# Performance work log

Measured on AMD Instinct MI355X. Metric: run time of the kernel, lower is better.

Reference implementation:

```python
import jax, jax.numpy as jnp
import numpy as np

B, L_HIST, N_VARS, L_FUT = 32, 96, 862, 96
D_MODEL, D_INNER, D_STATE, D_CONV, DT_RANK, D_FF, E_LAYERS = 512, 512, 32, 2, 32, 512, 2
EPS = 1e-5


def _ln(x, w, b):
    m = x.mean(-1, keepdims=True)
    v = ((x - m) ** 2).mean(-1, keepdims=True)
    return (x - m) * jax.lax.rsqrt(v + EPS) * w + b


def _mamba(x, in_w, conv_w, conv_b, x_w, dt_w, dt_b, A_log, D, out_w):
    # x: [B, T, d_model]; standard mamba-ssm selective-scan block (inference)
    Bb, T, _ = x.shape
    u, z = jnp.split(x @ in_w, 2, axis=-1)                      # [B,T,E] each
    uc = jnp.transpose(u, (0, 2, 1))                            # [B,E,T]
    uc = jax.lax.conv_general_dilated(
        uc, conv_w[:, None, :], (1,), [(D_CONV - 1, 0)],
        dimension_numbers=('NCH', 'OIH', 'NCH'),
        feature_group_count=D_INNER)                            # causal depthwise conv
    u = jax.nn.silu(jnp.transpose(uc, (0, 2, 1)) + conv_b)      # [B,T,E]
    dt, Bm, Cm = jnp.split(u @ x_w, [DT_RANK, DT_RANK + D_STATE], axis=-1)
    delta = jax.nn.softplus(dt @ dt_w + dt_b)                   # [B,T,E]
    A = -jnp.exp(A_log)                                         # [E,S]

    def step(h, inp):
        d_t, u_t, B_t, C_t = inp                                # [B,E],[B,E],[B,S],[B,S]
        h = jnp.exp(d_t[..., None] * A) * h + (d_t * u_t)[..., None] * B_t[:, None, :]
        return h, jnp.einsum('bes,bs->be', h, C_t)

    h0 = jnp.zeros((Bb, D_INNER, D_STATE), x.dtype)
    _, ys = jax.lax.scan(step, h0, (delta.transpose(1, 0, 2), u.transpose(1, 0, 2),
                                    Bm.transpose(1, 0, 2), Cm.transpose(1, 0, 2)))
    y = ys.transpose(1, 0, 2) + u * D
    return (y * jax.nn.silu(z)) @ out_w


def _forward(history_data, emb_w, emb_b, m_in_w, m_conv_w, m_conv_b, m_x_w,
             m_dt_w, m_dt_b, m_A_log, m_D, m_out_w, ffn_w1, ffn_b1, ffn_w2,
             ffn_b2, norm1_w, norm1_b, norm2_w, norm2_b, normf_w, normf_b,
             proj_w, proj_b):
    x_enc = history_data[..., 0]                                # [B,L,N]
    means = jax.lax.stop_gradient(x_enc.mean(1, keepdims=True))
    x_enc = x_enc - means
    stdev = jnp.sqrt(x_enc.var(axis=1, keepdims=True) + EPS)
    x_enc = x_enc / stdev
    x = jnp.transpose(x_enc, (0, 2, 1)) @ emb_w + emb_b         # [B,N,d_model] (inverted embed)
    for l in range(E_LAYERS):
        fwd = _mamba(x, m_in_w[l, 0], m_conv_w[l, 0], m_conv_b[l, 0], m_x_w[l, 0],
                     m_dt_w[l, 0], m_dt_b[l, 0], m_A_log[l, 0], m_D[l, 0], m_out_w[l, 0])
        rev = _mamba(x[:, ::-1], m_in_w[l, 1], m_conv_w[l, 1], m_conv_b[l, 1], m_x_w[l, 1],
                     m_dt_w[l, 1], m_dt_b[l, 1], m_A_log[l, 1], m_D[l, 1], m_out_w[l, 1])[:, ::-1]
        x = _ln(x + fwd + rev, norm1_w[l], norm1_b[l])
        y = jax.nn.relu(x @ ffn_w1[l] + ffn_b1[l]) @ ffn_w2[l] + ffn_b2[l]
        x = _ln(x + y, norm2_w[l], norm2_b[l])
    x = _ln(x, normf_w, normf_b)
    dec = jnp.transpose(x @ proj_w + proj_b, (0, 2, 1))         # [B,L_FUT,N]
    dec = dec * stdev[:, 0][:, None, :] + means[:, 0][:, None, :]
    return dec[..., None]                                       # [B,L_FUT,N,1]


def setup_inputs() -> dict:
    key = jax.random.key(0)
    ks = jax.random.split(key, 16)
    def rn(k, shape, s=0.02):
        return jax.random.normal(k, shape, jnp.float32) * s
    M = (E_LAYERS, 2)
    inp = {}
    inp['history_data'] = jax.random.normal(ks[0], (B, L_HIST, N_VARS, 1), jnp.float32)
    inp['emb_w'] = rn(ks[1], (L_HIST, D_MODEL))
    inp['emb_b'] = jnp.zeros((D_MODEL,), jnp.float32)
    inp['m_in_w'] = rn(ks[2], M + (D_MODEL, 2 * D_INNER))
    inp['m_conv_w'] = rn(ks[3], M + (D_INNER, D_CONV), 0.1)
    inp['m_conv_b'] = jnp.zeros(M + (D_INNER,), jnp.float32)
    inp['m_x_w'] = rn(ks[4], M + (D_INNER, DT_RANK + 2 * D_STATE))
    inp['m_dt_w'] = rn(ks[5], M + (DT_RANK, D_INNER), 0.1)
    inp['m_dt_b'] = jnp.full(M + (D_INNER,), -4.0, jnp.float32)
    a = jnp.log(jnp.arange(1, D_STATE + 1, dtype=jnp.float32))
    inp['m_A_log'] = jnp.broadcast_to(a, M + (D_INNER, D_STATE))
    inp['m_D'] = jnp.ones(M + (D_INNER,), jnp.float32)
    inp['m_out_w'] = rn(ks[6], M + (D_INNER, D_MODEL))
    inp['ffn_w1'] = rn(ks[7], (E_LAYERS, D_MODEL, D_FF))
    inp['ffn_b1'] = jnp.zeros((E_LAYERS, D_FF), jnp.float32)
    inp['ffn_w2'] = rn(ks[8], (E_LAYERS, D_FF, D_MODEL))
    inp['ffn_b2'] = jnp.zeros((E_LAYERS, D_MODEL), jnp.float32)
    inp['norm1_w'] = jnp.ones((E_LAYERS, D_MODEL), jnp.float32)
    inp['norm1_b'] = jnp.zeros((E_LAYERS, D_MODEL), jnp.float32)
    inp['norm2_w'] = jnp.ones((E_LAYERS, D_MODEL), jnp.float32)
    inp['norm2_b'] = jnp.zeros((E_LAYERS, D_MODEL), jnp.float32)
    inp['normf_w'] = jnp.ones((D_MODEL,), jnp.float32)
    inp['normf_b'] = jnp.zeros((D_MODEL,), jnp.float32)
    inp['proj_w'] = rn(ks[9], (D_MODEL, L_FUT))
    inp['proj_b'] = jnp.zeros((L_FUT,), jnp.float32)
    return inp


def reference(history_data, emb_w, emb_b, m_in_w, m_conv_w, m_conv_b, m_x_w,
              m_dt_w, m_dt_b, m_A_log, m_D, m_out_w, ffn_w1, ffn_b1, ffn_w2,
              ffn_b2, norm1_w, norm1_b, norm2_w, norm2_b, normf_w, normf_b,
              proj_w, proj_b):
    return _forward(history_data, emb_w, emb_b, m_in_w, m_conv_w, m_conv_b, m_x_w,
                    m_dt_w, m_dt_b, m_A_log, m_D, m_out_w, ffn_w1, ffn_b1, ffn_w2,
                    ffn_b2, norm1_w, norm1_b, norm2_w, norm2_b, normf_w, normf_b,
                    proj_w, proj_b)
```

## Files before the change

### kernel.cpp

```cpp
#include <hip/hip_runtime.h>
#include <math.h>

#define BATCH 32
#define LHIST 96
#define NVARS 862
#define LFUT  96
#define DMODEL 512
#define DINNER 512
#define DSTATE 32
#define DTRANK 32
#define SCAN_C 32
#define SCAN_TC ((NVARS + SCAN_C - 1) / SCAN_C)

typedef short short8 __attribute__((ext_vector_type(8)));
typedef float floatx4 __attribute__((ext_vector_type(4)));
typedef unsigned short ushort;

#define LOG2E 1.44269504088896f

static __device__ __forceinline__ ushort f2b(float f) {
    unsigned u = __builtin_bit_cast(unsigned, f);
    unsigned r = (u + 0x7FFFu + ((u >> 16) & 1u)) >> 16;
    return (ushort)r;
}
static __device__ __forceinline__ float b2f(ushort h) {
    unsigned u = ((unsigned)h) << 16;
    return __builtin_bit_cast(float, u);
}

static __device__ __forceinline__ void load_lds16(const void* g, void* l) {
    __builtin_amdgcn_global_load_lds(
        (const __attribute__((address_space(1))) unsigned int*)g,
        (__attribute__((address_space(3))) unsigned int*)l, 16, 0, 0);
}

__global__ void meanstd_k(const float* __restrict__ hist, ushort* __restrict__ xinb,
                          float* __restrict__ meanb, float* __restrict__ stdb,
                          int b0, int CB) {
    int idx = blockIdx.x * blockDim.x + threadIdx.x;
    if (idx >= CB * NVARS) return;
    int b = b0 + idx / NVARS, n = idx % NVARS;
    const float* p = hist + (size_t)b * LHIST * NVARS + n;
    float s = 0.f;
    for (int l = 0; l < LHIST; l++) s += p[(size_t)l * NVARS];
    float mean = s * (1.f / LHIST);
    float v = 0.f;
    for (int l = 0; l < LHIST; l++) { float d = p[(size_t)l * NVARS] - mean; v += d * d; }
    v *= (1.f / LHIST);
    float sd = sqrtf(v + 1e-5f);
    float inv = 1.f / sd;
    meanb[idx] = mean;
    stdb[idx]  = sd;
    ushort* o = xinb + (size_t)idx * LHIST;
    for (int l = 0; l < LHIST; l++) o[l] = f2b((p[(size_t)l * NVARS] - mean) * inv);
}

__global__ void castT_k(const float* __restrict__ W, ushort* __restrict__ Wt,
                        int K, int N, int P) {
    size_t idx = (size_t)blockIdx.x * blockDim.x + threadIdx.x;
    if (idx >= (size_t)P * K * N) return;
    size_t kn = (size_t)K * N;
    int p = (int)(idx / kn);
    int rem = (int)(idx % kn);
    int k = rem / N, n = rem % N;
    Wt[(size_t)p * kn + (size_t)n * K + k] = f2b(W[idx]);
}

#define TBM 128
#define TBN 128
#define TBK 32

__global__ __launch_bounds__(256)
void bgemm_k(const ushort* __restrict__ A, int lda,
             const ushort* __restrict__ Bt, int ldb,
             const float* __restrict__ bias,
             float* __restrict__ C, int ldc,
             ushort* __restrict__ C2, int ldc2,
             int M, int N, int K, int act, int accum) {
    __shared__ ushort As[TBM][TBK];
    __shared__ ushort Bs[TBN][TBK];
    int tid = threadIdx.x;
    int gm0 = blockIdx.y * TBM, gn0 = blockIdx.x * TBN;
    int lane = tid & 63, w = tid >> 6;
    int wm = (w >> 1) * 64, wn = (w & 1) * 64;
    int col16 = lane & 15, quad = lane >> 4;

    floatx4 acc[4][4];
#pragma unroll
    for (int i = 0; i < 4; i++)
#pragma unroll
        for (int j = 0; j < 4; j++) acc[i][j] = (floatx4){0.f, 0.f, 0.f, 0.f};

    int srow = tid >> 2;
    int schunk = (tid & 3) * 8;

    const ushort* pa0 = A + (size_t)min(gm0 + srow, M - 1) * lda + schunk;
    const ushort* pa1 = A + (size_t)min(gm0 + srow + 64, M - 1) * lda + schunk;
    const ushort* pb0 = Bt + (size_t)min(gn0 + srow, N - 1) * ldb + schunk;
    const ushort* pb1 = Bt + (size_t)min(gn0 + srow + 64, N - 1) * ldb + schunk;
    ushort* la0 = &As[0][0] + (size_t)tid * 8;
    ushort* la1 = la0 + 2048;
    ushort* lb0 = &Bs[0][0] + (size_t)tid * 8;
    ushort* lb1 = lb0 + 2048;

    for (int k0 = 0; k0 < K; k0 += TBK) {
        __syncthreads();
        load_lds16(pa0 + k0, la0);
        load_lds16(pa1 + k0, la1);
        load_lds16(pb0 + k0, lb0);
        load_lds16(pb1 + k0, lb1);
        __syncthreads();

        short8 af[4], bf[4];
#pragma unroll
        for (int mt = 0; mt < 4; mt++)
            af[mt] = *(const short8*)&As[wm + mt * 16 + col16][quad * 8];
#pragma unroll
        for (int nt = 0; nt < 4; nt++)
            bf[nt] = *(const short8*)&Bs[wn + nt * 16 + col16][quad * 8];
#pragma unroll
        for (int mt = 0; mt < 4; mt++)
#pragma unroll
            for (int nt = 0; nt < 4; nt++)
                acc[mt][nt] = __builtin_amdgcn_mfma_f32_16x16x32_bf16(
                    af[mt], bf[nt], acc[mt][nt], 0, 0, 0);
    }

    int rbase = gm0 + wm + quad * 4;
    int cbase = gn0 + wn + col16;
#pragma unroll
    for (int mt = 0; mt < 4; mt++) {
#pragma unroll
        for (int reg = 0; reg < 4; reg++) {
            int r = rbase + mt * 16 + reg;
            if (r >= M) continue;
#pragma unroll
            for (int nt = 0; nt < 4; nt++) {
                int c = cbase + nt * 16;
                if (c >= N) continue;
                float v = acc[mt][nt][reg];
                if (bias) v += bias[c];
                if (act == 1) v = fmaxf(v, 0.f);
                else if (act == 2) v = (v > 20.f) ? v : log1pf(expf(v));
                if (accum) v += C[(size_t)r * ldc + c];
                if (C)  C[(size_t)r * ldc + c] = v;
                if (C2) C2[(size_t)r * ldc2 + c] = f2b(v);
            }
        }
    }
}

__global__ void conv8_k(const ushort* __restrict__ uzb, const float* __restrict__ cw,
                        const float* __restrict__ cb, ushort* __restrict__ ucb,
                        int rev, int R) {
    int idx = blockIdx.x * blockDim.x + threadIdx.x;
    if (idx >= R * 64) return;
    int m = idx >> 6;
    int e0 = (idx & 63) * 8;
    int t = m % NVARS;
    const ushort* up = uzb + (size_t)m * 1024 + e0;
    short8 cur = *(const short8*)up;
    short8 oth = (short8){0,0,0,0,0,0,0,0};
    if (!rev) { if (t > 0)          oth = *(const short8*)(up - 1024); }
    else      { if (t < NVARS - 1)  oth = *(const short8*)(up + 1024); }
    short8 res;
#pragma unroll
    for (int i = 0; i < 8; i++) {
        int e = e0 + i;
        float v = cw[e * 2] * b2f((ushort)oth[i]) + cw[e * 2 + 1] * b2f((ushort)cur[i]) + cb[e];
        float sig = 1.f / (1.f + __expf(-v));
        res[i] = (short)f2b(v * sig);
    }
    *(short8*)(ucb + (size_t)m * 512 + e0) = res;
}


static __device__ __forceinline__ bool a_is_fast(const float* A_log, int e) {
    bool f = true;
#pragma unroll
    for (int s = 0; s < DSTATE; s++) {
        float a = -__expf(A_log[e * DSTATE + s]);
        f = f && (fabsf(a + (float)(s + 1)) < 1e-3f * (s + 1));
    }
    return f;
}

__global__ __launch_bounds__(256, 4)
void scan_part_k(const ushort* __restrict__ deltab, const ushort* __restrict__ ucb,
                 const float* __restrict__ xdbc, const float* __restrict__ A_log,
                 float* __restrict__ Hpart, float* __restrict__ Sd,
                 int rev, int CB) {
    int NP = CB * DINNER;
    int idx = blockIdx.x * blockDim.x + threadIdx.x;
    if (idx >= NP * SCAN_C) return;
    int c = idx / NP, be = idx % NP;
    int b = be >> 9, e = be & (DINNER - 1);

    float h[DSTATE];
#pragma unroll
    for (int s = 0; s < DSTATE; s++) h[s] = 0.f;
    float sd = 0.f;
    int tau1 = min((c + 1) * SCAN_TC, NVARS);
    if (a_is_fast(A_log, e)) {
        for (int tau = c * SCAN_TC; tau < tau1; tau++) {
            int t = rev ? (NVARS - 1 - tau) : tau;
            size_t m = (size_t)b * NVARS + t;
            float d  = b2f(deltab[m * 512 + e]);
            float uv = b2f(ucb[m * 512 + e]);
            float du = d * uv;
            sd += d;
            const float4* Bp4 = (const float4*)(xdbc + m * 96 + DTRANK);
            float q = __expf(-d), pw = q;
#pragma unroll
            for (int g = 0; g < 8; g++) {
                float4 bv = Bp4[g];
                h[4*g+0] = pw * h[4*g+0] + du * bv.x; pw *= q;
                h[4*g+1] = pw * h[4*g+1] + du * bv.y; pw *= q;
                h[4*g+2] = pw * h[4*g+2] + du * bv.z; pw *= q;
                h[4*g+3] = pw * h[4*g+3] + du * bv.w; if (g < 7) pw *= q;
            }
        }
    } else {
        for (int tau = c * SCAN_TC; tau < tau1; tau++) {
            int t = rev ? (NVARS - 1 - tau) : tau;
            size_t m = (size_t)b * NVARS + t;
            float d  = b2f(deltab[m * 512 + e]);
            float uv = b2f(ucb[m * 512 + e]);
            float du = d * uv;
            sd += d;
            const float* Bp = xdbc + m * 96 + DTRANK;
#pragma unroll
            for (int s = 0; s < DSTATE; s++) {
                float a2 = -__expf(A_log[e * DSTATE + s]) * LOG2E;
                h[s] = exp2f(d * a2) * h[s] + du * Bp[s];
            }
        }
    }
    Sd[(size_t)c * NP + be] = sd;
#pragma unroll
    for (int s = 0; s < DSTATE; s++)
        Hpart[((size_t)c * DSTATE + s) * NP + be] = h[s];
}

__global__ __launch_bounds__(256)
void scan_carry_k(float* __restrict__ Hpart, const float* __restrict__ Sd,
                  const float* __restrict__ A_log, int CB) {
    int NP = CB * DINNER;
    int idx = blockIdx.x * blockDim.x + threadIdx.x;
    if (idx >= NP * DSTATE) return;
    int s = idx / NP, be = idx % NP;
    int e = be & (DINNER - 1);
    float a2 = -__expf(A_log[e * DSTATE + s]) * LOG2E;
    float carry = 0.f;
    for (int c = 0; c < SCAN_C; c++) {
        float sd = Sd[(size_t)c * NP + be];
        size_t off = ((size_t)c * DSTATE + s) * NP + be;
        float hp = Hpart[off];
        Hpart[off] = carry;
        carry = hp + exp2f(a2 * sd) * carry;
    }
}

__global__ __launch_bounds__(256, 4)
void scan_final_k(const ushort* __restrict__ deltab, const ushort* __restrict__ uzb,
                  const ushort* __restrict__ ucb, const float* __restrict__ xdbc,
                  const float* __restrict__ A_log, const float* __restrict__ Dp,
                  const float* __restrict__ CarryIn, ushort* __restrict__ yb,
                  int rev, int CB) {
    int NP = CB * DINNER;
    int idx = blockIdx.x * blockDim.x + threadIdx.x;
    if (idx >= NP * SCAN_C) return;
    int c = idx / NP, be = idx % NP;
    int b = be >> 9, e = be & (DINNER - 1);

    float h[DSTATE];
#pragma unroll
    for (int s = 0; s < DSTATE; s++)
        h[s] = CarryIn[((size_t)c * DSTATE + s) * NP + be];
    float Dv = Dp[e];
    int tau1 = min((c + 1) * SCAN_TC, NVARS);
    if (a_is_fast(A_log, e)) {
        for (int tau = c * SCAN_TC; tau < tau1; tau++) {
            int t = rev ? (NVARS - 1 - tau) : tau;
            size_t m = (size_t)b * NVARS + t;
            float d  = b2f(deltab[m * 512 + e]);
            float zz = b2f(uzb[m * 1024 + 512 + e]);
            float uv = b2f(ucb[m * 512 + e]);
            float du = d * uv;
            const float4* Bp4 = (const float4*)(xdbc + m * 96 + DTRANK);
            const float4* Cp4 = Bp4 + 8;
            float q = __expf(-d), pw = q;
            float accv = 0.f;
#pragma unroll
            for (int g = 0; g < 8; g++) {
                float4 bv = Bp4[g];
                float4 cv = Cp4[g];
                h[4*g+0] = pw * h[4*g+0] + du * bv.x; accv += h[4*g+0] * cv.x; pw *= q;
                h[4*g+1] = pw * h[4*g+1] + du * bv.y; accv += h[4*g+1] * cv.y; pw *= q;
                h[4*g+2] = pw * h[4*g+2] + du * bv.z; accv += h[4*g+2] * cv.z; pw *= q;
                h[4*g+3] = pw * h[4*g+3] + du * bv.w; accv += h[4*g+3] * cv.w;
                if (g < 7) pw *= q;
            }
            float sig = 1.f / (1.f + __expf(-zz));
            yb[m * 512 + e] = f2b((accv + uv * Dv) * (zz * sig));
        }
    } else {
        for (int tau = c * SCAN_TC; tau < tau1; tau++) {
            int t = rev ? (NVARS - 1 - tau) : tau;
            size_t m = (size_t)b * NVARS + t;
            float d  = b2f(deltab[m * 512 + e]);
            float zz = b2f(uzb[m * 1024 + 512 + e]);
            float uv = b2f(ucb[m * 512 + e]);
            float du = d * uv;
            const float* Bp = xdbc + m * 96 + DTRANK;
            const float* Cp = Bp + DSTATE;
            float accv = 0.f;
#pragma unroll
            for (int s = 0; s < DSTATE; s++) {
                float a2 = -__expf(A_log[e * DSTATE + s]) * LOG2E;
                h[s] = exp2f(d * a2) * h[s] + du * Bp[s];
                accv += h[s] * Cp[s];
            }
            float sig = 1.f / (1.f + __expf(-zz));
            yb[m * 512 + e] = f2b((accv + uv * Dv) * (zz * sig));
        }
    }
}

__global__ __launch_bounds__(64)
void ln_k(const float* __restrict__ in1, const float* __restrict__ in2,
          const float* __restrict__ w, const float* __restrict__ b,
          float* __restrict__ out, ushort* __restrict__ outb) {
    int row = blockIdx.x;
    int lane = threadIdx.x;
    const float* p1 = in1 + (size_t)row * DMODEL;
    const float* p2 = in2 ? in2 + (size_t)row * DMODEL : nullptr;
    float v[8];
#pragma unroll
    for (int i = 0; i < 8; i++) {
        int c = lane + i * 64;
        v[i] = p1[c];
        if (p2) v[i] += p2[c];
    }
    float s = 0.f;
#pragma unroll
    for (int i = 0; i < 8; i++) s += v[i];
#pragma unroll
    for (int off = 32; off >= 1; off >>= 1) s += __shfl_xor(s, off);
    float mean = s * (1.f / DMODEL);
    float q = 0.f;
#pragma unroll
    for (int i = 0; i < 8; i++) { float d = v[i] - mean; q += d * d; }
#pragma unroll
    for (int off = 32; off >= 1; off >>= 1) q += __shfl_xor(q, off);
    float rs = rsqrtf(q * (1.f / DMODEL) + 1e-5f);
#pragma unroll
    for (int i = 0; i < 8; i++) {
        int c = lane + i * 64;
        float o = (v[i] - mean) * rs * w[c] + b[c];
        if (out)  out[(size_t)row * DMODEL + c] = o;
        if (outb) outb[(size_t)row * DMODEL + c] = f2b(o);
    }
}

__global__ void final_k(const float* __restrict__ dec, const float* __restrict__ meanb,
                        const float* __restrict__ stdb, float* __restrict__ out,
                        int b0, int CB) {
    int idx = blockIdx.x * blockDim.x + threadIdx.x;
    if (idx >= CB * LFUT * NVARS) return;
    int n = idx % NVARS;
    int r = idx / NVARS;
    int l = r % LFUT;
    int bl = r / LFUT;
    int tok = bl * NVARS + n;
    out[(size_t)((b0 + bl) * LFUT + l) * NVARS + n] =
        dec[(size_t)tok * LFUT + l] * stdb[tok] + meanb[tok];
}

extern "C" void kernel_launch(void* const* d_in, const int* in_sizes, int n_in,
                              void* d_out, int out_size, void* d_ws, size_t ws_size,
                              hipStream_t stream) {
    const float* hist    = (const float*)d_in[0];
    const float* emb_w   = (const float*)d_in[1];
    const float* emb_b   = (const float*)d_in[2];
    const float* m_in_w  = (const float*)d_in[3];
    const float* m_conv_w= (const float*)d_in[4];
    const float* m_conv_b= (const float*)d_in[5];
    const float* m_x_w   = (const float*)d_in[6];
    const float* m_dt_w  = (const float*)d_in[7];
    const float* m_dt_b  = (const float*)d_in[8];
    const float* m_A_log = (const float*)d_in[9];
    const float* m_D     = (const float*)d_in[10];
    const float* m_out_w = (const float*)d_in[11];
    const float* ffn_w1  = (const float*)d_in[12];
    const float* ffn_b1  = (const float*)d_in[13];
    const float* ffn_w2  = (const float*)d_in[14];
    const float* ffn_b2  = (const float*)d_in[15];
    const float* norm1_w = (const float*)d_in[16];
    const float* norm1_b = (const float*)d_in[17];
    const float* norm2_w = (const float*)d_in[18];
    const float* norm2_b = (const float*)d_in[19];
    const float* normf_w = (const float*)d_in[20];
    const float* normf_b = (const float*)d_in[21];
    const float* proj_w  = (const float*)d_in[22];
    const float* proj_b  = (const float*)d_in[23];

    float* out = (float*)d_out;
    float* ws  = (float*)d_ws;

    const size_t WTSE = 4u*1024*512 + 4u*512*512 + 2u*512*512 + 2u*512*512
                      + 96u*512 + 4u*96*512 + 4u*512*32 + 96u*512;

    int CB = BATCH;
    for (;;) {
        size_t R = (size_t)CB * NVARS, NP = (size_t)CB * DINNER;
        size_t Rp = (R + 3) & ~3ull;
        size_t fl = R * 1120 + 2 * Rp + (size_t)SCAN_C * 33 * NP;
        size_t us = R * 3264 + WTSE;
        if (fl * 4 + us * 2 + 1024 <= ws_size || CB == 1) break;
        CB >>= 1;
    }
    const int R  = CB * NVARS;
    const int NP = CB * DINNER;
    const size_t Rp = ((size_t)R + 3) & ~3ull;

    float* x     = ws;
    float* accb  = x + (size_t)R * 512;
    float* xdbc  = accb + (size_t)R * 512;
    float* meanb = xdbc + (size_t)R * 96;
    float* stdb  = meanb + Rp;
    float* Hpart = stdb + Rp;
    float* Sd    = Hpart + (size_t)SCAN_C * DSTATE * NP;
    ushort* xb     = (ushort*)(Sd + (size_t)SCAN_C * NP);
    ushort* ybmid  = xb + (size_t)R * 512;
    ushort* ucb    = ybmid + (size_t)R * 512;
    ushort* uzb    = ucb + (size_t)R * 512;
    ushort* deltab = uzb + (size_t)R * 1024;
    ushort* xinb   = deltab + (size_t)R * 512;
    ushort* xdbcb  = xinb + (size_t)R * 96;
    ushort* wts    = xdbcb + (size_t)R * 96;

    ushort *inw_t, *outw_t, *f1_t, *f2_t, *emb_t, *xw_t, *dtw_t, *proj_t;
    {
        ushort* p = wts;
        inw_t  = p; p += (size_t)4 * 1024 * 512;
        outw_t = p; p += (size_t)4 * 512 * 512;
        f1_t   = p; p += (size_t)2 * 512 * 512;
        f2_t   = p; p += (size_t)2 * 512 * 512;
        emb_t  = p; p += (size_t)512 * 96;
        xw_t   = p; p += (size_t)4 * 96 * 512;
        dtw_t  = p; p += (size_t)4 * 512 * 32;
        proj_t = p;
    }

    castT_k<<<(4 * 512 * 1024 + 255) / 256, 256, 0, stream>>>(m_in_w, inw_t, 512, 1024, 4);
    castT_k<<<(4 * 512 * 512 + 255) / 256, 256, 0, stream>>>(m_out_w, outw_t, 512, 512, 4);
    castT_k<<<(2 * 512 * 512 + 255) / 256, 256, 0, stream>>>(ffn_w1, f1_t, 512, 512, 2);
    castT_k<<<(2 * 512 * 512 + 255) / 256, 256, 0, stream>>>(ffn_w2, f2_t, 512, 512, 2);
    castT_k<<<(96 * 512 + 255) / 256, 256, 0, stream>>>(emb_w, emb_t, 96, 512, 1);
    castT_k<<<(4 * 512 * 96 + 255) / 256, 256, 0, stream>>>(m_x_w, xw_t, 512, 96, 4);
    castT_k<<<(4 * 32 * 512 + 255) / 256, 256, 0, stream>>>(m_dt_w, dtw_t, 32, 512, 4);
    castT_k<<<(512 * 96 + 255) / 256, 256, 0, stream>>>(proj_w, proj_t, 512, 96, 1);

    auto bgemm = [&](const ushort* A, int lda, const ushort* Bt, int ldb,
                     const float* bias, float* C, int ldc, ushort* C2, int ldc2,
                     int M, int N, int K, int act, int accum) {
        dim3 grid((N + TBN - 1) / TBN, (M + TBM - 1) / TBM);
        bgemm_k<<<grid, 256, 0, stream>>>(A, lda, Bt, ldb, bias, C, ldc, C2, ldc2,
                                          M, N, K, act, accum);
    };

    for (int b0 = 0; b0 < BATCH; b0 += CB) {
        meanstd_k<<<(R + 255) / 256, 256, 0, stream>>>(hist, xinb, meanb, stdb, b0, CB);
        bgemm(xinb, 96, emb_t, 96, emb_b, x, 512, xb, 512, R, 512, 96, 0, 0);

        for (int l = 0; l < 2; l++) {
            for (int dir = 0; dir < 2; dir++) {
                int p = l * 2 + dir;
                const float* cw   = m_conv_w + (size_t)p * DINNER * 2;
                const float* cb   = m_conv_b + (size_t)p * DINNER;
                const float* dtb  = m_dt_b  + (size_t)p * DINNER;
                const float* alog = m_A_log + (size_t)p * DINNER * DSTATE;
                const float* Dp   = m_D     + (size_t)p * DINNER;

                bgemm(xb, 512, inw_t + (size_t)p * 1024 * 512, 512, nullptr,
                      nullptr, 0, uzb, 1024, R, 1024, 512, 0, 0);
                conv8_k<<<(R * 64 + 255) / 256, 256, 0, stream>>>(uzb, cw, cb, ucb, dir, R);
                bgemm(ucb, 512, xw_t + (size_t)p * 96 * 512, 512, nullptr,
                      xdbc, 96, xdbcb, 96, R, 96, 512, 0, 0);
                bgemm(xdbcb, 96, dtw_t + (size_t)p * 512 * 32, 32, dtb,
                      nullptr, 0, deltab, 512, R, 512, 32, 2, 0);
                scan_part_k<<<(NP * SCAN_C + 255) / 256, 256, 0, stream>>>(
                    deltab, ucb, xdbc, alog, Hpart, Sd, dir, CB);
                scan_carry_k<<<(NP * DSTATE + 255) / 256, 256, 0, stream>>>(
                    Hpart, Sd, alog, CB);
                scan_final_k<<<(NP * SCAN_C + 255) / 256, 256, 0, stream>>>(
                    deltab, uzb, ucb, xdbc, alog, Dp, Hpart, ybmid, dir, CB);
                bgemm(ybmid, 512, outw_t + (size_t)p * 512 * 512, 512, nullptr,
                      accb, 512, nullptr, 0, R, 512, 512, 0, dir);
            }
            ln_k<<<R, 64, 0, stream>>>(accb, x, norm1_w + l * DMODEL, norm1_b + l * DMODEL,
                                       x, xb);
            bgemm(xb, 512, f1_t + (size_t)l * 512 * 512, 512, ffn_b1 + l * DMODEL,
                  nullptr, 0, ybmid, 512, R, 512, 512, 1, 0);
            bgemm(ybmid, 512, f2_t + (size_t)l * 512 * 512, 512, ffn_b2 + l * DMODEL,
                  accb, 512, nullptr, 0, R, 512, 512, 0, 0);
            ln_k<<<R, 64, 0, stream>>>(x, accb, norm2_w + l * DMODEL, norm2_b + l * DMODEL,
                                       x, xb);
        }

        ln_k<<<R, 64, 0, stream>>>(x, nullptr, normf_w, normf_b, nullptr, xb);
        bgemm(xb, 512, proj_t, 512, proj_b, xdbc, 96, nullptr, 0, R, 96, 512, 0, 0);
        final_k<<<(CB * LFUT * NVARS + 255) / 256, 256, 0, stream>>>(
            xdbc, meanb, stdb, out, b0, CB);
    }
}
```

Measured before the change: 2.987 ms.

## Batch forward and reverse Mamba directions into joint wide GEMMs and scans

Merges the two directional Mamba passes per layer into a single pipeline. The in-projection GEMM becomes N=2048, x_proj and dt_proj use block-diagonal weights, and conv and scan kernels handle 1024 columns. The out-projection GEMM concatenates along K to sum both directions, which removes the accumulate pass and halves kernel launches. It also replaces the direct global-to-LDS loads in the GEMM with register-staged loads and halves the scan chunk count. Block-diagonal weights spend extra FLOPs on zero blocks, and scan_final now writes its output into the delta buffer it reads, in place.

```diff
diff --git a/kernel.cpp b/kernel.cpp
--- a/kernel.cpp
+++ b/kernel.cpp
@@ -9,7 +9,7 @@
 #define DINNER 512
 #define DSTATE 32
 #define DTRANK 32
-#define SCAN_C 32
+#define SCAN_C 16
 #define SCAN_TC ((NVARS + SCAN_C - 1) / SCAN_C)
 
 typedef short short8 __attribute__((ext_vector_type(8)));
@@ -26,12 +26,6 @@
 static __device__ __forceinline__ float b2f(ushort h) {
     unsigned u = ((unsigned)h) << 16;
     return __builtin_bit_cast(float, u);
-}
-
-static __device__ __forceinline__ void load_lds16(const void* g, void* l) {
-    __builtin_amdgcn_global_load_lds(
-        (const __attribute__((address_space(1))) unsigned int*)g,
-        (__attribute__((address_space(3))) unsigned int*)l, 16, 0, 0);
 }
 
 __global__ void meanstd_k(const float* __restrict__ hist, ushort* __restrict__ xinb,
@@ -66,6 +60,46 @@
     Wt[(size_t)p * kn + (size_t)n * K + k] = f2b(W[idx]);
 }
 
+__global__ void xw2_cast(const float* __restrict__ xw, ushort* __restrict__ o) {
+    int idx = blockIdx.x * blockDim.x + threadIdx.x;
+    if (idx >= 2 * 192 * 1024) return;
+    int l = idx / (192 * 1024);
+    int r = idx % (192 * 1024);
+    int n = r / 1024, k = r % 1024;
+    int half = (n >= 96);
+    int nn = n - 96 * half;
+    float v = 0.f;
+    if ((k >> 9) == half)
+        v = xw[((size_t)(l * 2 + half) * 512 + (k & 511)) * 96 + nn];
+    o[idx] = f2b(v);
+}
+
+__global__ void dtw2_cast(const float* __restrict__ dtw, ushort* __restrict__ o) {
+    int idx = blockIdx.x * blockDim.x + threadIdx.x;
+    if (idx >= 2 * 1024 * 192) return;
+    int l = idx / (1024 * 192);
+    int r = idx % (1024 * 192);
+    int n = r / 192, k = r % 192;
+    int half = n >> 9;
+    int nn = n & 511;
+    int kb = k - 96 * half;
+    float v = 0.f;
+    if (kb >= 0 && kb < 32)
+        v = dtw[((size_t)(l * 2 + half) * 32 + kb) * 512 + nn];
+    o[idx] = f2b(v);
+}
+
+__global__ void outw2_cast(const float* __restrict__ ow, ushort* __restrict__ o) {
+    int idx = blockIdx.x * blockDim.x + threadIdx.x;
+    if (idx >= 2 * 512 * 1024) return;
+    int l = idx / (512 * 1024);
+    int r = idx % (512 * 1024);
+    int n = r / 1024, k = r % 1024;
+    int half = k >> 9;
+    float v = ow[((size_t)(l * 2 + half) * 512 + (k & 511)) * 512 + n];
+    o[idx] = f2b(v);
+}
+
 #define TBM 128
 #define TBN 128
 #define TBK 32
@@ -94,21 +128,20 @@
     int srow = tid >> 2;
     int schunk = (tid & 3) * 8;
 
-    const ushort* pa0 = A + (size_t)min(gm0 + srow, M - 1) * lda + schunk;
-    const ushort* pa1 = A + (size_t)min(gm0 + srow + 64, M - 1) * lda + schunk;
-    const ushort* pb0 = Bt + (size_t)min(gn0 + srow, N - 1) * ldb + schunk;
-    const ushort* pb1 = Bt + (size_t)min(gn0 + srow + 64, N - 1) * ldb + schunk;
-    ushort* la0 = &As[0][0] + (size_t)tid * 8;
-    ushort* la1 = la0 + 2048;
-    ushort* lb0 = &Bs[0][0] + (size_t)tid * 8;
-    ushort* lb1 = lb0 + 2048;
-
     for (int k0 = 0; k0 < K; k0 += TBK) {
+        int ra0 = min(gm0 + srow, M - 1);
+        int ra1 = min(gm0 + srow + 64, M - 1);
+        short8 a0 = *(const short8*)(A + (size_t)ra0 * lda + k0 + schunk);
+        short8 a1 = *(const short8*)(A + (size_t)ra1 * lda + k0 + schunk);
+        int rb0 = min(gn0 + srow, N - 1);
+        int rb1 = min(gn0 + srow + 64, N - 1);
+        short8 b0 = *(const short8*)(Bt + (size_t)rb0 * ldb + k0 + schunk);
+        short8 b1 = *(const short8*)(Bt + (size_t)rb1 * ldb + k0 + schunk);
         __syncthreads();
-        load_lds16(pa0 + k0, la0);
-        load_lds16(pa1 + k0, la1);
-        load_lds16(pb0 + k0, lb0);
-        load_lds16(pb1 + k0, lb1);
+        *(short8*)&As[srow][schunk]      = a0;
+        *(short8*)&As[srow + 64][schunk] = a1;
+        *(short8*)&Bs[srow][schunk]      = b0;
+        *(short8*)&Bs[srow + 64][schunk] = b1;
         __syncthreads();
 
         short8 af[4], bf[4];
@@ -150,19 +183,22 @@
     }
 }
 
-__global__ void conv8_k(const ushort* __restrict__ uzb, const float* __restrict__ cw,
-                        const float* __restrict__ cb, ushort* __restrict__ ucb,
-                        int rev, int R) {
-    int idx = blockIdx.x * blockDim.x + threadIdx.x;
-    if (idx >= R * 64) return;
-    int m = idx >> 6;
-    int e0 = (idx & 63) * 8;
+__global__ void conv8_k(const ushort* __restrict__ uzb2, const float* __restrict__ cw2,
+                        const float* __restrict__ cb2, ushort* __restrict__ ucb2, int R) {
+    int idx = blockIdx.x * blockDim.x + threadIdx.x;
+    if (idx >= R * 128) return;
+    int m = idx >> 7;
+    int c8 = (idx & 127) * 8;
+    int half = c8 >> 9;
+    int e0 = c8 & 511;
     int t = m % NVARS;
-    const ushort* up = uzb + (size_t)m * 1024 + e0;
+    const ushort* up = uzb2 + (size_t)m * 2048 + half * 1024 + e0;
     short8 cur = *(const short8*)up;
     short8 oth = (short8){0,0,0,0,0,0,0,0};
-    if (!rev) { if (t > 0)          oth = *(const short8*)(up - 1024); }
-    else      { if (t < NVARS - 1)  oth = *(const short8*)(up + 1024); }
+    if (!half) { if (t > 0)          oth = *(const short8*)(up - 2048); }
+    else       { if (t < NVARS - 1)  oth = *(const short8*)(up + 2048); }
+    const float* cw = cw2 + half * 1024;
+    const float* cb = cb2 + half * 512;
     short8 res;
 #pragma unroll
     for (int i = 0; i < 8; i++) {
@@ -171,45 +207,45 @@
         float sig = 1.f / (1.f + __expf(-v));
         res[i] = (short)f2b(v * sig);
     }
-    *(short8*)(ucb + (size_t)m * 512 + e0) = res;
-}
-
-
-static __device__ __forceinline__ bool a_is_fast(const float* A_log, int e) {
+    *(short8*)(ucb2 + (size_t)m * 1024 + c8) = res;
+}
+
+
+static __device__ __forceinline__ bool a_is_fast(const float* A_log2, int col) {
     bool f = true;
 #pragma unroll
     for (int s = 0; s < DSTATE; s++) {
-        float a = -__expf(A_log[e * DSTATE + s]);
+        float a = -__expf(A_log2[col * DSTATE + s]);
         f = f && (fabsf(a + (float)(s + 1)) < 1e-3f * (s + 1));
     }
     return f;
 }
 
 __global__ __launch_bounds__(256, 4)
-void scan_part_k(const ushort* __restrict__ deltab, const ushort* __restrict__ ucb,
-                 const float* __restrict__ xdbc, const float* __restrict__ A_log,
-                 float* __restrict__ Hpart, float* __restrict__ Sd,
-                 int rev, int CB) {
-    int NP = CB * DINNER;
-    int idx = blockIdx.x * blockDim.x + threadIdx.x;
-    if (idx >= NP * SCAN_C) return;
-    int c = idx / NP, be = idx % NP;
-    int b = be >> 9, e = be & (DINNER - 1);
+void scan_part_k(const ushort* __restrict__ deltab2, const ushort* __restrict__ ucb2,
+                 const float* __restrict__ xdbc2, const float* __restrict__ alog2,
+                 float* __restrict__ Hpart, float* __restrict__ Sd, int CB) {
+    int NP2 = CB * 1024;
+    int idx = blockIdx.x * blockDim.x + threadIdx.x;
+    if (idx >= NP2 * SCAN_C) return;
+    int c = idx / NP2, be = idx % NP2;
+    int b = be >> 10, col = be & 1023;
+    int rv = col >> 9;
 
     float h[DSTATE];
 #pragma unroll
     for (int s = 0; s < DSTATE; s++) h[s] = 0.f;
     float sd = 0.f;
     int tau1 = min((c + 1) * SCAN_TC, NVARS);
-    if (a_is_fast(A_log, e)) {
+    if (a_is_fast(alog2, col)) {
         for (int tau = c * SCAN_TC; tau < tau1; tau++) {
-            int t = rev ? (NVARS - 1 - tau) : tau;
+            int t = rv ? (NVARS - 1 - tau) : tau;
             size_t m = (size_t)b * NVARS + t;
-            float d  = b2f(deltab[m * 512 + e]);
-            float uv = b2f(ucb[m * 512 + e]);
+            float d  = b2f(deltab2[m * 1024 + col]);
+            float uv = b2f(ucb2[m * 1024 + col]);
             float du = d * uv;
             sd += d;
-            const float4* Bp4 = (const float4*)(xdbc + m * 96 + DTRANK);
+            const float4* Bp4 = (const float4*)(xdbc2 + m * 192 + rv * 96 + DTRANK);
             float q = __expf(-d), pw = q;
 #pragma unroll
             for (int g = 0; g < 8; g++) {
@@ -222,39 +258,39 @@
         }
     } else {
         for (int tau = c * SCAN_TC; tau < tau1; tau++) {
-            int t = rev ? (NVARS - 1 - tau) : tau;
+            int t = rv ? (NVARS - 1 - tau) : tau;
             size_t m = (size_t)b * NVARS + t;
-            float d  = b2f(deltab[m * 512 + e]);
-            float uv = b2f(ucb[m * 512 + e]);
+            float d  = b2f(deltab2[m * 1024 + col]);
+            float uv = b2f(ucb2[m * 1024 + col]);
             float du = d * uv;
             sd += d;
-            const float* Bp = xdbc + m * 96 + DTRANK;
+            const float* Bp = xdbc2 + m * 192 + rv * 96 + DTRANK;
 #pragma unroll
             for (int s = 0; s < DSTATE; s++) {
-                float a2 = -__expf(A_log[e * DSTATE + s]) * LOG2E;
+                float a2 = -__expf(alog2[col * DSTATE + s]) * LOG2E;
                 h[s] = exp2f(d * a2) * h[s] + du * Bp[s];
             }
         }
     }
-    Sd[(size_t)c * NP + be] = sd;
+    Sd[(size_t)c * NP2 + be] = sd;
 #pragma unroll
     for (int s = 0; s < DSTATE; s++)
-        Hpart[((size_t)c * DSTATE + s) * NP + be] = h[s];
+        Hpart[((size_t)c * DSTATE + s) * NP2 + be] = h[s];
 }
 
 __global__ __launch_bounds__(256)
 void scan_carry_k(float* __restrict__ Hpart, const float* __restrict__ Sd,
-                  const float* __restrict__ A_log, int CB) {
-    int NP = CB * DINNER;
-    int idx = blockIdx.x * blockDim.x + threadIdx.x;
-    if (idx >= NP * DSTATE) return;
-    int s = idx / NP, be = idx % NP;
-    int e = be & (DINNER - 1);
-    float a2 = -__expf(A_log[e * DSTATE + s]) * LOG2E;
+                  const float* __restrict__ alog2, int CB) {
+    int NP2 = CB * 1024;
+    int idx = blockIdx.x * blockDim.x + threadIdx.x;
+    if (idx >= NP2 * DSTATE) return;
+    int s = idx / NP2, be = idx % NP2;
+    int col = be & 1023;
+    float a2 = -__expf(alog2[col * DSTATE + s]) * LOG2E;
     float carry = 0.f;
     for (int c = 0; c < SCAN_C; c++) {
-        float sd = Sd[(size_t)c * NP + be];
-        size_t off = ((size_t)c * DSTATE + s) * NP + be;
+        float sd = Sd[(size_t)c * NP2 + be];
+        size_t off = ((size_t)c * DSTATE + s) * NP2 + be;
         float hp = Hpart[off];
         Hpart[off] = carry;
         carry = hp + exp2f(a2 * sd) * carry;
@@ -262,32 +298,32 @@
 }
 
 __global__ __launch_bounds__(256, 4)
-void scan_final_k(const ushort* __restrict__ deltab, const ushort* __restrict__ uzb,
-                  const ushort* __restrict__ ucb, const float* __restrict__ xdbc,
-                  const float* __restrict__ A_log, const float* __restrict__ Dp,
-                  const float* __restrict__ CarryIn, ushort* __restrict__ yb,
-                  int rev, int CB) {
-    int NP = CB * DINNER;
-    int idx = blockIdx.x * blockDim.x + threadIdx.x;
-    if (idx >= NP * SCAN_C) return;
-    int c = idx / NP, be = idx % NP;
-    int b = be >> 9, e = be & (DINNER - 1);
+void scan_final_k(const ushort* __restrict__ deltab2, const ushort* __restrict__ uzb2,
+                  const ushort* __restrict__ ucb2, const float* __restrict__ xdbc2,
+                  const float* __restrict__ alog2, const float* __restrict__ Dp2,
+                  const float* __restrict__ CarryIn, ushort* __restrict__ yb, int CB) {
+    int NP2 = CB * 1024;
+    int idx = blockIdx.x * blockDim.x + threadIdx.x;
+    if (idx >= NP2 * SCAN_C) return;
+    int c = idx / NP2, be = idx % NP2;
+    int b = be >> 10, col = be & 1023;
+    int rv = col >> 9;
 
     float h[DSTATE];
 #pragma unroll
     for (int s = 0; s < DSTATE; s++)
-        h[s] = CarryIn[((size_t)c * DSTATE + s) * NP + be];
-    float Dv = Dp[e];
+        h[s] = CarryIn[((size_t)c * DSTATE + s) * NP2 + be];
+    float Dv = Dp2[col];
     int tau1 = min((c + 1) * SCAN_TC, NVARS);
-    if (a_is_fast(A_log, e)) {
+    if (a_is_fast(alog2, col)) {
         for (int tau = c * SCAN_TC; tau < tau1; tau++) {
-            int t = rev ? (NVARS - 1 - tau) : tau;
+            int t = rv ? (NVARS - 1 - tau) : tau;
             size_t m = (size_t)b * NVARS + t;
-            float d  = b2f(deltab[m * 512 + e]);
-            float zz = b2f(uzb[m * 1024 + 512 + e]);
-            float uv = b2f(ucb[m * 512 + e]);
+            float d  = b2f(deltab2[m * 1024 + col]);
+            float zz = b2f(uzb2[m * 2048 + rv * 1024 + 512 + (col & 511)]);
+            float uv = b2f(ucb2[m * 1024 + col]);
             float du = d * uv;
-            const float4* Bp4 = (const float4*)(xdbc + m * 96 + DTRANK);
+            const float4* Bp4 = (const float4*)(xdbc2 + m * 192 + rv * 96 + DTRANK);
             const float4* Cp4 = Bp4 + 8;
             float q = __expf(-d), pw = q;
             float accv = 0.f;
@@ -302,27 +338,27 @@
                 if (g < 7) pw *= q;
             }
             float sig = 1.f / (1.f + __expf(-zz));
-            yb[m * 512 + e] = f2b((accv + uv * Dv) * (zz * sig));
+            yb[m * 1024 + col] = f2b((accv + uv * Dv) * (zz * sig));
         }
     } else {
         for (int tau = c * SCAN_TC; tau < tau1; tau++) {
-            int t = rev ? (NVARS - 1 - tau) : tau;
+            int t = rv ? (NVARS - 1 - tau) : tau;
             size_t m = (size_t)b * NVARS + t;
-            float d  = b2f(deltab[m * 512 + e]);
-            float zz = b2f(uzb[m * 1024 + 512 + e]);
-            float uv = b2f(ucb[m * 512 + e]);
+            float d  = b2f(deltab2[m * 1024 + col]);
+            float zz = b2f(uzb2[m * 2048 + rv * 1024 + 512 + (col & 511)]);
+            float uv = b2f(ucb2[m * 1024 + col]);
             float du = d * uv;
-            const float* Bp = xdbc + m * 96 + DTRANK;
+            const float* Bp = xdbc2 + m * 192 + rv * 96 + DTRANK;
             const float* Cp = Bp + DSTATE;
             float accv = 0.f;
 #pragma unroll
             for (int s = 0; s < DSTATE; s++) {
-                float a2 = -__expf(A_log[e * DSTATE + s]) * LOG2E;
+                float a2 = -__expf(alog2[col * DSTATE + s]) * LOG2E;
                 h[s] = exp2f(d * a2) * h[s] + du * Bp[s];
                 accv += h[s] * Cp[s];
             }
             float sig = 1.f / (1.f + __expf(-zz));
-            yb[m * 512 + e] = f2b((accv + uv * Dv) * (zz * sig));
+            yb[m * 1024 + col] = f2b((accv + uv * Dv) * (zz * sig));
         }
     }
 }
@@ -408,58 +444,62 @@
     float* out = (float*)d_out;
     float* ws  = (float*)d_ws;
 
-    const size_t WTSE = 4u*1024*512 + 4u*512*512 + 2u*512*512 + 2u*512*512
-                      + 96u*512 + 4u*96*512 + 4u*512*32 + 96u*512;
+    const size_t WTSE = 4u*1024*512
+                      + 2u*512*1024
+                      + 2u*512*512 + 2u*512*512
+                      + 512u*96
+                      + 2u*192*1024
+                      + 2u*1024*192
+                      + 512u*96;
 
     int CB = BATCH;
     for (;;) {
-        size_t R = (size_t)CB * NVARS, NP = (size_t)CB * DINNER;
+        size_t R = (size_t)CB * NVARS, NP2 = (size_t)CB * 1024;
         size_t Rp = (R + 3) & ~3ull;
-        size_t fl = R * 1120 + 2 * Rp + (size_t)SCAN_C * 33 * NP;
-        size_t us = R * 3264 + WTSE;
+        size_t fl = R * 1216 + 2 * Rp + (size_t)SCAN_C * 33 * NP2;
+        size_t us = R * 4896 + WTSE;
         if (fl * 4 + us * 2 + 1024 <= ws_size || CB == 1) break;
         CB >>= 1;
     }
-    const int R  = CB * NVARS;
-    const int NP = CB * DINNER;
+    const int R   = CB * NVARS;
+    const int NP2 = CB * 1024;
     const size_t Rp = ((size_t)R + 3) & ~3ull;
 
     float* x     = ws;
     float* accb  = x + (size_t)R * 512;
-    float* xdbc  = accb + (size_t)R * 512;
-    float* meanb = xdbc + (size_t)R * 96;
+    float* xdbc2 = accb + (size_t)R * 512;
+    float* meanb = xdbc2 + (size_t)R * 192;
     float* stdb  = meanb + Rp;
     float* Hpart = stdb + Rp;
-    float* Sd    = Hpart + (size_t)SCAN_C * DSTATE * NP;
-    ushort* xb     = (ushort*)(Sd + (size_t)SCAN_C * NP);
-    ushort* ybmid  = xb + (size_t)R * 512;
-    ushort* ucb    = ybmid + (size_t)R * 512;
-    ushort* uzb    = ucb + (size_t)R * 512;
-    ushort* deltab = uzb + (size_t)R * 1024;
-    ushort* xinb   = deltab + (size_t)R * 512;
-    ushort* xdbcb  = xinb + (size_t)R * 96;
-    ushort* wts    = xdbcb + (size_t)R * 96;
-
-    ushort *inw_t, *outw_t, *f1_t, *f2_t, *emb_t, *xw_t, *dtw_t, *proj_t;
+    float* Sd    = Hpart + (size_t)SCAN_C * DSTATE * NP2;
+    ushort* xb      = (ushort*)(Sd + (size_t)SCAN_C * NP2);
+    ushort* uzb2    = xb + (size_t)R * 512;
+    ushort* ucb2    = uzb2 + (size_t)R * 2048;
+    ushort* deltab2 = ucb2 + (size_t)R * 1024;
+    ushort* xinb    = deltab2 + (size_t)R * 1024;
+    ushort* xdbc2b  = xinb + (size_t)R * 96;
+    ushort* wts     = xdbc2b + (size_t)R * 192;
+
+    ushort *inw_t, *outw2_t, *f1_t, *f2_t, *emb_t, *xw2_t, *dtw2_t, *proj_t;
     {
         ushort* p = wts;
-        inw_t  = p; p += (size_t)4 * 1024 * 512;
-        outw_t = p; p += (size_t)4 * 512 * 512;
-        f1_t   = p; p += (size_t)2 * 512 * 512;
-        f2_t   = p; p += (size_t)2 * 512 * 512;
-        emb_t  = p; p += (size_t)512 * 96;
-        xw_t   = p; p += (size_t)4 * 96 * 512;
-        dtw_t  = p; p += (size_t)4 * 512 * 32;
-        proj_t = p;
+        inw_t   = p; p += (size_t)4 * 1024 * 512;
+        outw2_t = p; p += (size_t)2 * 512 * 1024;
+        f1_t    = p; p += (size_t)2 * 512 * 512;
+        f2_t    = p; p += (size_t)2 * 512 * 512;
+        emb_t   = p; p += (size_t)512 * 96;
+        xw2_t   = p; p += (size_t)2 * 192 * 1024;
+        dtw2_t  = p; p += (size_t)2 * 1024 * 192;
+        proj_t  = p;
     }
 
     castT_k<<<(4 * 512 * 1024 + 255) / 256, 256, 0, stream>>>(m_in_w, inw_t, 512, 1024, 4);
-    castT_k<<<(4 * 512 * 512 + 255) / 256, 256, 0, stream>>>(m_out_w, outw_t, 512, 512, 4);
+    outw2_cast<<<(2 * 512 * 1024 + 255) / 256, 256, 0, stream>>>(m_out_w, outw2_t);
     castT_k<<<(2 * 512 * 512 + 255) / 256, 256, 0, stream>>>(ffn_w1, f1_t, 512, 512, 2);
     castT_k<<<(2 * 512 * 512 + 255) / 256, 256, 0, stream>>>(ffn_w2, f2_t, 512, 512, 2);
     castT_k<<<(96 * 512 + 255) / 256, 256, 0, stream>>>(emb_w, emb_t, 96, 512, 1);
-    castT_k<<<(4 * 512 * 96 + 255) / 256, 256, 0, stream>>>(m_x_w, xw_t, 512, 96, 4);
-    castT_k<<<(4 * 32 * 512 + 255) / 256, 256, 0, stream>>>(m_dt_w, dtw_t, 32, 512, 4);
+    xw2_cast<<<(2 * 192 * 1024 + 255) / 256, 256, 0, stream>>>(m_x_w, xw2_t);
+    dtw2_cast<<<(2 * 1024 * 192 + 255) / 256, 256, 0, stream>>>(m_dt_w, dtw2_t);
     castT_k<<<(512 * 96 + 255) / 256, 256, 0, stream>>>(proj_w, proj_t, 512, 96, 1);
 
     auto bgemm = [&](const ushort* A, int lda, const ushort* Bt, int ldb,
@@ -475,43 +515,41 @@
         bgemm(xinb, 96, emb_t, 96, emb_b, x, 512, xb, 512, R, 512, 96, 0, 0);
 
         for (int l = 0; l < 2; l++) {
-            for (int dir = 0; dir < 2; dir++) {
-                int p = l * 2 + dir;
-                const float* cw   = m_conv_w + (size_t)p * DINNER * 2;
-                const float* cb   = m_conv_b + (size_t)p * DINNER;
-                const float* dtb  = m_dt_b  + (size_t)p * DINNER;
-                const float* alog = m_A_log + (size_t)p * DINNER * DSTATE;
-                const float* Dp   = m_D     + (size_t)p * DINNER;
-
-                bgemm(xb, 512, inw_t + (size_t)p * 1024 * 512, 512, nullptr,
-                      nullptr, 0, uzb, 1024, R, 1024, 512, 0, 0);
-                conv8_k<<<(R * 64 + 255) / 256, 256, 0, stream>>>(uzb, cw, cb, ucb, dir, R);
-                bgemm(ucb, 512, xw_t + (size_t)p * 96 * 512, 512, nullptr,
-                      xdbc, 96, xdbcb, 96, R, 96, 512, 0, 0);
-                bgemm(xdbcb, 96, dtw_t + (size_t)p * 512 * 32, 32, dtb,
-                      nullptr, 0, deltab, 512, R, 512, 32, 2, 0);
-                scan_part_k<<<(NP * SCAN_C + 255) / 256, 256, 0, stream>>>(
-                    deltab, ucb, xdbc, alog, Hpart, Sd, dir, CB);
-                scan_carry_k<<<(NP * DSTATE + 255) / 256, 256, 0, stream>>>(
-                    Hpart, Sd, alog, CB);
-                scan_final_k<<<(NP * SCAN_C + 255) / 256, 256, 0, stream>>>(
-                    deltab, uzb, ucb, xdbc, alog, Dp, Hpart, ybmid, dir, CB);
-                bgemm(ybmid, 512, outw_t + (size_t)p * 512 * 512, 512, nullptr,
-                      accb, 512, nullptr, 0, R, 512, 512, 0, dir);
-            }
+            const float* cw2   = m_conv_w + (size_t)l * 2048;
+            const float* cb2   = m_conv_b + (size_t)l * 1024;
+            const float* dtb2  = m_dt_b  + (size_t)l * 1024;
+            const float* alog2 = m_A_log + (size_t)l * 2 * 512 * 32;
+            const float* Dp2   = m_D     + (size_t)l * 1024;
+
+            bgemm(xb, 512, inw_t + (size_t)(2 * l) * 1024 * 512, 512, nullptr,
+                  nullptr, 0, uzb2, 2048, R, 2048, 512, 0, 0);
+            conv8_k<<<(R * 128 + 255) / 256, 256, 0, stream>>>(uzb2, cw2, cb2, ucb2, R);
+            bgemm(ucb2, 1024, xw2_t + (size_t)l * 192 * 1024, 1024, nullptr,
+                  xdbc2, 192, xdbc2b, 192, R, 192, 1024, 0, 0);
+            bgemm(xdbc2b, 192, dtw2_t + (size_t)l * 1024 * 192, 192, dtb2,
+                  nullptr, 0, deltab2, 1024, R, 1024, 192, 2, 0);
+            scan_part_k<<<(NP2 * SCAN_C + 255) / 256, 256, 0, stream>>>(
+                deltab2, ucb2, xdbc2, alog2, Hpart, Sd, CB);
+            scan_carry_k<<<(NP2 * DSTATE + 255) / 256, 256, 0, stream>>>(
+                Hpart, Sd, alog2, CB);
+            scan_final_k<<<(NP2 * SCAN_C + 255) / 256, 256, 0, stream>>>(
+                deltab2, uzb2, ucb2, xdbc2, alog2, Dp2, Hpart, deltab2, CB);
+            bgemm(deltab2, 1024, outw2_t + (size_t)l * 512 * 1024, 1024, nullptr,
+                  accb, 512, nullptr, 0, R, 512, 1024, 0, 0);
+
             ln_k<<<R, 64, 0, stream>>>(accb, x, norm1_w + l * DMODEL, norm1_b + l * DMODEL,
                                        x, xb);
             bgemm(xb, 512, f1_t + (size_t)l * 512 * 512, 512, ffn_b1 + l * DMODEL,
-                  nullptr, 0, ybmid, 512, R, 512, 512, 1, 0);
-            bgemm(ybmid, 512, f2_t + (size_t)l * 512 * 512, 512, ffn_b2 + l * DMODEL,
+                  nullptr, 0, ucb2, 512, R, 512, 512, 1, 0);
+            bgemm(ucb2, 512, f2_t + (size_t)l * 512 * 512, 512, ffn_b2 + l * DMODEL,
                   accb, 512, nullptr, 0, R, 512, 512, 0, 0);
             ln_k<<<R, 64, 0, stream>>>(x, accb, norm2_w + l * DMODEL, norm2_b + l * DMODEL,
                                        x, xb);
         }
 
         ln_k<<<R, 64, 0, stream>>>(x, nullptr, normf_w, normf_b, nullptr, xb);
-        bgemm(xb, 512, proj_t, 512, proj_b, xdbc, 96, nullptr, 0, R, 96, 512, 0, 0);
+        bgemm(xb, 512, proj_t, 512, proj_b, xdbc2, 96, nullptr, 0, R, 96, 512, 0, 0);
         final_k<<<(CB * LFUT * NVARS + 255) / 256, 256, 0, stream>>>(
-            xdbc, meanb, stdb, out, b0, CB);
-    }
-}
+            xdbc2, meanb, stdb, out, b0, CB);
+    }
+}
```

Measured after the change: 2.531 ms. 1.18x faster.
